# Kernel tuning notes

Measured on AMD Instinct MI355X. Metric: run time of the kernel, lower is better.

## Reference

```python
import jax, jax.numpy as jnp
import numpy as np

B, S, HID = 1, 4096, 2048
H, KVH, D = 16, 8, 128
EPS = 1e-6
SCALE = D ** -0.5


def rms_norm(x, w):
    # normalize over last axis in float32, per-head weight of size D
    xf = x.astype(jnp.float32)
    var = jnp.mean(xf * xf, axis=-1, keepdims=True)
    return (w * xf * jax.lax.rsqrt(var + EPS)).astype(x.dtype)


def rotate_half(x):
    x1, x2 = jnp.split(x, 2, axis=-1)
    return jnp.concatenate([-x2, x1], axis=-1)


def setup_inputs() -> dict:
    key = jax.random.key(0)
    ks = jax.random.split(key, 12)
    x = jax.random.normal(ks[0], (B, S, HID), jnp.float32)
    # RoPE tables
    inv_freq = 1.0 / (10000.0 ** (jnp.arange(0, D, 2, dtype=jnp.float32) / D))
    t = jnp.arange(S, dtype=jnp.float32)
    freqs = jnp.outer(t, inv_freq)                       # [S, D/2]
    emb = jnp.concatenate([freqs, freqs], axis=-1)       # [S, D]
    cos, sin = jnp.cos(emb), jnp.sin(emb)
    # causal additive mask
    neg = jnp.finfo(jnp.float32).min
    mask = jnp.where(jnp.tril(jnp.ones((S, S), bool)), 0.0, neg)[None, None]
    sc = 0.02
    Wq = jax.random.normal(ks[1], (H * D, HID), jnp.float32) * sc
    bq = jnp.zeros((H * D,), jnp.float32)
    Wk = jax.random.normal(ks[2], (KVH * D, HID), jnp.float32) * sc
    bk = jnp.zeros((KVH * D,), jnp.float32)
    Wv = jax.random.normal(ks[3], (KVH * D, HID), jnp.float32) * sc
    bv = jnp.zeros((KVH * D,), jnp.float32)
    Wo = jax.random.normal(ks[4], (HID, H * D), jnp.float32) * sc
    qn_w = jnp.ones((D,), jnp.float32)
    kn_w = jnp.ones((D,), jnp.float32)
    return {"x": x, "cos": cos, "sin": sin, "mask": mask,
            "Wq": Wq, "bq": bq, "Wk": Wk, "bk": bk, "Wv": Wv, "bv": bv,
            "Wo": Wo, "qn_w": qn_w, "kn_w": kn_w}


def reference(x, cos, sin, mask, Wq, bq, Wk, bk, Wv, bv, Wo, qn_w, kn_w):
    b, s, _ = x.shape
    q = (x @ Wq.T + bq).reshape(b, s, H, D)
    k = (x @ Wk.T + bk).reshape(b, s, KVH, D)
    v = (x @ Wv.T + bv).reshape(b, s, KVH, D)
    q = rms_norm(q, qn_w)
    k = rms_norm(k, kn_w)
    # RoPE: cos/sin [S, D] broadcast over batch and head dims
    c = cos[None, :, None, :]
    sn = sin[None, :, None, :]
    q = q * c + rotate_half(q) * sn
    k = k * c + rotate_half(k) * sn
    # GQA: repeat kv heads (repeat_interleave along head axis)
    reps = H // KVH
    k = jnp.repeat(k, reps, axis=2)
    v = jnp.repeat(v, reps, axis=2)
    # [b, H, s, d]
    q = q.transpose(0, 2, 1, 3)
    k = k.transpose(0, 2, 1, 3)
    v = v.transpose(0, 2, 1, 3)
    scores = jnp.einsum('bhqd,bhkd->bhqk', q, k) * SCALE + mask
    attn = jax.nn.softmax(scores.astype(jnp.float32), axis=-1).astype(q.dtype)
    out = jnp.einsum('bhqk,bhkd->bhqd', attn, v)
    out = out.transpose(0, 2, 1, 3).reshape(b, s, H * D)
    return out @ Wo.T
```

## Files before the change

kernel.cpp:

```cpp
#include <hip/hip_runtime.h>
#include <hip/hip_bf16.h>
#include <stdint.h>

#define S_LEN 4096
#define HID 2048
#define NH 16
#define KVH 8
#define DH 128
#define EPS 1e-6f
#define SCALE 0.08838834764831845f
#define LOG2E 1.4426950408889634f

#if __has_builtin(__builtin_amdgcn_exp2f)
#define EXP2(x) __builtin_amdgcn_exp2f(x)
#else
#define EXP2(x) exp2f(x)
#endif

typedef __bf16 bf16x8 __attribute__((ext_vector_type(8)));
typedef __bf16 bf16x4 __attribute__((ext_vector_type(4)));
typedef float f32x4 __attribute__((ext_vector_type(4)));

__device__ inline void gl_lds16(const __bf16* g, __bf16* l) {
  __builtin_amdgcn_global_load_lds(
      (const __attribute__((address_space(1))) void*)g,
      (__attribute__((address_space(3))) void*)l, 16, 0, 0);
}

__global__ __launch_bounds__(256) void f2b4(
    const float* __restrict__ in, __bf16* __restrict__ out, int n4) {
  int i = blockIdx.x * 256 + threadIdx.x;
  if (i < n4) {
    float4 v = ((const float4*)in)[i];
    bf16x4 o;
    o[0] = (__bf16)v.x; o[1] = (__bf16)v.y; o[2] = (__bf16)v.z; o[3] = (__bf16)v.w;
    ((bf16x4*)out)[i] = o;
  }
}


template <typename TC>
__global__ __launch_bounds__(256) void gemm128(
    const __bf16* __restrict__ A, const __bf16* __restrict__ B,
    const float* __restrict__ bias, TC* __restrict__ C,
    int N, int K, int bias_mode)
{
  __shared__ __attribute__((aligned(16))) __bf16 As[3][128 * 32];
  __shared__ __attribute__((aligned(16))) __bf16 Bs[3][128 * 32];
  const int wave = threadIdx.x >> 6, lane = threadIdx.x & 63;
  const int quad = lane >> 4, l16 = lane & 15;
  const int wm = wave >> 1, wn = wave & 1;
  const int m0 = blockIdx.y * 128, n0 = blockIdx.x * 128;
  const int srow = lane >> 2, scol = (lane & 3) * 8;

  auto stage = [&](int buf, int k0) {
#pragma unroll
    for (int j = wave; j < 8; j += 4) {
      gl_lds16(A + (size_t)(m0 + j * 16 + srow) * K + k0 + scol, &As[buf][j * 512]);
      gl_lds16(B + (size_t)(n0 + j * 16 + srow) * K + k0 + scol, &Bs[buf][j * 512]);
    }
  };

  f32x4 acc[4][4] = {};
  const int nk = K >> 5;
  stage(0, 0);
  stage(1, 32);

  int cur = 0, pre = 2;
  for (int kt = 0; kt < nk; ++kt) {
    if (kt + 1 < nk) asm volatile("s_waitcnt vmcnt(4)" ::: "memory");
    else             asm volatile("s_waitcnt vmcnt(0)" ::: "memory");
    __builtin_amdgcn_s_barrier();
    __builtin_amdgcn_sched_barrier(0);
    if (kt + 2 < nk) stage(pre, (kt + 2) * 32);

    bf16x8 af[4], bfr[4];
#pragma unroll
    for (int s = 0; s < 4; ++s) {
      af[s]  = *(const bf16x8*)(&As[cur][(wm * 64 + s * 16 + l16) * 32 + quad * 8]);
      bfr[s] = *(const bf16x8*)(&Bs[cur][(wn * 64 + s * 16 + l16) * 32 + quad * 8]);
    }
#pragma unroll
    for (int ms = 0; ms < 4; ++ms)
#pragma unroll
      for (int ns = 0; ns < 4; ++ns)
        acc[ms][ns] = __builtin_amdgcn_mfma_f32_16x16x32_bf16(
            af[ms], bfr[ns], acc[ms][ns], 0, 0, 0);

    cur = (cur == 2) ? 0 : cur + 1;
    pre = (pre == 2) ? 0 : pre + 1;
  }

#pragma unroll
  for (int ms = 0; ms < 4; ++ms)
#pragma unroll
    for (int ns = 0; ns < 4; ++ns)
#pragma unroll
      for (int r = 0; r < 4; ++r) {
        int row = m0 + wm * 64 + ms * 16 + quad * 4 + r;
        int col = n0 + wn * 64 + ns * 16 + l16;
        float v = acc[ms][ns][r];
        if (bias_mode == 1) v += bias[col];
        else if (bias_mode == 2) v += bias[row];
        C[(size_t)row * N + col] = (TC)v;
      }
}

__global__ __launch_bounds__(256) void gemm_qkv(
    const __bf16* __restrict__ A,
    const __bf16* __restrict__ B,
    const float* __restrict__ bq, const float* __restrict__ bk,
    const float* __restrict__ bv,
    __bf16* __restrict__ qo,
    __bf16* __restrict__ ko,
    __bf16* __restrict__ vto)
{
  __shared__ __attribute__((aligned(16))) __bf16 As[3][128 * 32];
  __shared__ __attribute__((aligned(16))) __bf16 Bs[3][128 * 32];
  const int wave = threadIdx.x >> 6, lane = threadIdx.x & 63;
  const int quad = lane >> 4, l16 = lane & 15;
  const int wm = wave >> 1, wn = wave & 1;
  const int m0 = blockIdx.y * 128, n0 = blockIdx.x * 128;
  const int srow = lane >> 2, scol = (lane & 3) * 8;
  const int K = HID;

  auto stage = [&](int buf, int k0) {
#pragma unroll
    for (int j = wave; j < 8; j += 4) {
      gl_lds16(A + (size_t)(m0 + j * 16 + srow) * K + k0 + scol, &As[buf][j * 512]);
      gl_lds16(B + (size_t)(n0 + j * 16 + srow) * K + k0 + scol, &Bs[buf][j * 512]);
    }
  };

  f32x4 acc[4][4] = {};
  const int nk = K >> 5;
  stage(0, 0);
  stage(1, 32);

  int cur = 0, pre = 2;
  for (int kt = 0; kt < nk; ++kt) {
    if (kt + 1 < nk) asm volatile("s_waitcnt vmcnt(4)" ::: "memory");
    else             asm volatile("s_waitcnt vmcnt(0)" ::: "memory");
    __builtin_amdgcn_s_barrier();
    __builtin_amdgcn_sched_barrier(0);
    if (kt + 2 < nk) stage(pre, (kt + 2) * 32);

    bf16x8 af[4], bfr[4];
#pragma unroll
    for (int s = 0; s < 4; ++s) {
      af[s]  = *(const bf16x8*)(&As[cur][(wm * 64 + s * 16 + l16) * 32 + quad * 8]);
      bfr[s] = *(const bf16x8*)(&Bs[cur][(wn * 64 + s * 16 + l16) * 32 + quad * 8]);
    }
#pragma unroll
    for (int ms = 0; ms < 4; ++ms)
#pragma unroll
      for (int ns = 0; ns < 4; ++ns)
        acc[ms][ns] = __builtin_amdgcn_mfma_f32_16x16x32_bf16(
            af[ms], bfr[ns], acc[ms][ns], 0, 0, 0);

    cur = (cur == 2) ? 0 : cur + 1;
    pre = (pre == 2) ? 0 : pre + 1;
  }

  if (blockIdx.x < 24) {
#pragma unroll
    for (int ms = 0; ms < 4; ++ms)
#pragma unroll
      for (int ns = 0; ns < 4; ++ns)
#pragma unroll
        for (int r = 0; r < 4; ++r) {
          int row = m0 + wm * 64 + ms * 16 + quad * 4 + r;
          int col = n0 + wn * 64 + ns * 16 + l16;
          float v = acc[ms][ns][r];
          if (col < 2048) { v += bq[col];        qo[(size_t)row * HID + col] = (__bf16)v; }
          else            { v += bk[col - 2048]; ko[(size_t)row * (KVH * DH) + (col - 2048)] = (__bf16)v; }
        }
  } else {
#pragma unroll
    for (int ms = 0; ms < 4; ++ms)
#pragma unroll
      for (int ns = 0; ns < 4; ++ns) {
        int vr = n0 - 3072 + wn * 64 + ns * 16 + l16;
        int s0 = m0 + wm * 64 + ms * 16 + quad * 4;
        float b = bv[vr];
        bf16x4 p;
#pragma unroll
        for (int r = 0; r < 4; ++r) p[r] = (__bf16)(acc[ms][ns][r] + b);
        *(bf16x4*)(vto + (size_t)vr * S_LEN + s0) = p;
      }
  }
}

__global__ __launch_bounds__(256) void rmsnorm_rope(
    __bf16* __restrict__ q, __bf16* __restrict__ k,
    const float* __restrict__ cosb, const float* __restrict__ sinb,
    const float* __restrict__ qw, const float* __restrict__ kw)
{
  const int wave = threadIdx.x >> 6;
  const int lane = threadIdx.x & 63;
  const int row = blockIdx.x * 4 + wave;
  const int s   = row / (NH + KVH);
  const int idx = row % (NH + KVH);

  __bf16* base;
  const float* w;
  float oscale;
  if (idx < NH) { base = q + ((size_t)s * NH + idx) * DH;         w = qw; oscale = SCALE * LOG2E; }
  else          { base = k + ((size_t)s * KVH + (idx - NH)) * DH; w = kw; oscale = 1.0f; }

  float x1 = (float)base[lane];
  float x2 = (float)base[lane + 64];
  float ss = x1 * x1 + x2 * x2;
#pragma unroll
  for (int m = 1; m < 64; m <<= 1) ss += __shfl_xor(ss, m, 64);
  float inv = rsqrtf(ss * (1.0f / 128.0f) + EPS);

  float xh1 = x1 * inv * w[lane];
  float xh2 = x2 * inv * w[lane + 64];
  const float* cs = cosb + (size_t)s * DH;
  const float* sn = sinb + (size_t)s * DH;
  base[lane]      = (__bf16)((xh1 * cs[lane]      - xh2 * sn[lane])      * oscale);
  base[lane + 64] = (__bf16)((xh2 * cs[lane + 64] + xh1 * sn[lane + 64]) * oscale);
}

__global__ __launch_bounds__(256) void attn2(
    const __bf16* __restrict__ q,
    const __bf16* __restrict__ k,
    const __bf16* __restrict__ vt,
    __bf16* __restrict__ o)
{
  __shared__ __attribute__((aligned(16))) __bf16 Ks[2][64 * DH];
  __shared__ __attribute__((aligned(16))) __bf16 Vs[2][DH * 64];
  __shared__ __attribute__((aligned(16))) __bf16 pl[4][16 * 72];
  const int wave = threadIdx.x >> 6, lane = threadIdx.x & 63;
  const int quad = lane >> 4, l16 = lane & 15;
  const int h = blockIdx.y, kvh = h >> 1;

  const __bf16* kh = k + (size_t)kvh * DH;
  const __bf16* vh = vt + (size_t)kvh * DH * S_LEN;

  int krow[4], kcol[4], vrow[4], vcol[4];
#pragma unroll
  for (int i = 0; i < 4; ++i) {
    int j = wave + i * 4;
    int r = j * 4 + (lane >> 4);
    int cbK = ((lane & 15) * 16) ^ ((r & 7) << 4);
    krow[i] = r; kcol[i] = cbK >> 1;
    int d = j * 8 + (lane >> 3);
    int cbV = ((lane & 7) * 16) ^ ((d & 7) << 4);
    vrow[i] = d; vcol[i] = cbV >> 1;
  }
  auto stage = [&](int buf, int k0) {
#pragma unroll
    for (int i = 0; i < 4; ++i)
      gl_lds16(kh + (size_t)(k0 + krow[i]) * (KVH * DH) + kcol[i],
               &Ks[buf][(wave + i * 4) * 512]);
#pragma unroll
    for (int i = 0; i < 4; ++i)
      gl_lds16(vh + (size_t)vrow[i] * S_LEN + k0 + vcol[i],
               &Vs[buf][(wave + i * 4) * 512]);
  };

  for (int phase = 0; phase < 2; ++phase) {
    const int qt = phase == 0 ? (int)blockIdx.x : 63 - (int)blockIdx.x;
    const int qbase = qt * 64 + wave * 16;

    bf16x8 qa[4];
    const __bf16* qrow = q + ((size_t)(qbase + l16) * NH + h) * DH + quad * 8;
#pragma unroll
    for (int c = 0; c < 4; ++c) qa[c] = *(const bf16x8*)(qrow + c * 32);

    f32x4 oacc[8] = {};
    float mrun[4], lrun[4];
#pragma unroll
    for (int r = 0; r < 4; ++r) { mrun[r] = -3.0e38f; lrun[r] = 0.0f; }

    __syncthreads();
    stage(0, 0);

    for (int kt = 0; kt <= qt; ++kt) {
      const int cur = kt & 1;
      const int k0 = kt * 64;
      __syncthreads();
      if (kt < qt) stage(cur ^ 1, k0 + 64);

      const char* ksb = (const char*)Ks[cur];
      const char* vsb = (const char*)Vs[cur];

      f32x4 sc[4] = {};
#pragma unroll
      for (int tt = 0; tt < 4; ++tt) {
        const int row = tt * 16 + l16;
        const int swz = (row & 7) << 4;
#pragma unroll
        for (int c = 0; c < 4; ++c) {
          bf16x8 bk = *(const bf16x8*)(ksb + row * 256 + ((c * 64 + quad * 16) ^ swz));
          sc[tt] = __builtin_amdgcn_mfma_f32_16x16x32_bf16(qa[c], bk, sc[tt], 0, 0, 0);
        }
      }
      if (kt == qt) {
#pragma unroll
        for (int tt = 0; tt < 4; ++tt)
#pragma unroll
          for (int r = 0; r < 4; ++r) {
            int col = k0 + tt * 16 + l16;
            int row = qbase + quad * 4 + r;
            if (col > row) sc[tt][r] = -3.0e38f;
          }
      }
      float pmax[4];
      bool defer = true;
#pragma unroll
      for (int r = 0; r < 4; ++r) {
        float mx = fmaxf(fmaxf(sc[0][r], sc[1][r]), fmaxf(sc[2][r], sc[3][r]));
        pmax[r] = mx;
        defer = defer && (mx - mrun[r] <= 8.0f);
      }
      if (__all(defer)) {
#pragma unroll
        for (int r = 0; r < 4; ++r) {
          float s0 = EXP2(sc[0][r] - mrun[r]);
          float s1 = EXP2(sc[1][r] - mrun[r]);
          float s2 = EXP2(sc[2][r] - mrun[r]);
          float s3 = EXP2(sc[3][r] - mrun[r]);
          sc[0][r] = s0; sc[1][r] = s1; sc[2][r] = s2; sc[3][r] = s3;
          lrun[r] += (s0 + s1) + (s2 + s3);
        }
      } else {
#pragma unroll
        for (int r = 0; r < 4; ++r) {
          float mx = pmax[r];
#pragma unroll
          for (int msk = 1; msk < 16; msk <<= 1) mx = fmaxf(mx, __shfl_xor(mx, msk, 64));
          float mnew = fmaxf(mrun[r], mx);
          float sum = 0.0f;
#pragma unroll
          for (int tt = 0; tt < 4; ++tt) {
            float p = EXP2(sc[tt][r] - mnew);
            sc[tt][r] = p;
            sum += p;
          }
          float alpha = EXP2(mrun[r] - mnew);
          lrun[r] = lrun[r] * alpha + sum;
          mrun[r] = mnew;
#pragma unroll
          for (int c = 0; c < 8; ++c) oacc[c][r] *= alpha;
        }
      }
#pragma unroll
      for (int tt = 0; tt < 4; ++tt)
#pragma unroll
        for (int r = 0; r < 4; ++r)
          pl[wave][(quad * 4 + r) * 72 + tt * 16 + l16] = (__bf16)sc[tt][r];
      bf16x8 pa[2];
#pragma unroll
      for (int kc = 0; kc < 2; ++kc)
        pa[kc] = *(const bf16x8*)(pl[wave] + l16 * 72 + kc * 32 + quad * 8);
#pragma unroll
      for (int c = 0; c < 8; ++c)
#pragma unroll
        for (int kc = 0; kc < 2; ++kc) {
          const int d = c * 16 + l16;
          bf16x8 bv = *(const bf16x8*)(
              vsb + d * 128 + ((kc * 64 + quad * 16) ^ ((d & 7) << 4)));
          oacc[c] = __builtin_amdgcn_mfma_f32_16x16x32_bf16(pa[kc], bv, oacc[c], 0, 0, 0);
        }
    }

#pragma unroll
    for (int r = 0; r < 4; ++r) {
#pragma unroll
      for (int msk = 1; msk < 16; msk <<= 1) lrun[r] += __shfl_xor(lrun[r], msk, 64);
      lrun[r] = 1.0f / lrun[r];
    }
#pragma unroll
    for (int c = 0; c < 8; ++c)
#pragma unroll
      for (int r = 0; r < 4; ++r) {
        int row = qbase + quad * 4 + r;
        o[((size_t)row * NH + h) * DH + c * 16 + l16] = (__bf16)(oacc[c][r] * lrun[r]);
      }
  }
}

extern "C" void kernel_launch(void* const* d_in, const int* in_sizes, int n_in,
                              void* d_out, int out_size, void* d_ws, size_t ws_size,
                              hipStream_t stream) {
  const float* x    = (const float*)d_in[0];
  const float* cosb = (const float*)d_in[1];
  const float* sinb = (const float*)d_in[2];
  const float* Wq  = (const float*)d_in[4];
  const float* bq  = (const float*)d_in[5];
  const float* Wk  = (const float*)d_in[6];
  const float* bk  = (const float*)d_in[7];
  const float* Wv  = (const float*)d_in[8];
  const float* bv  = (const float*)d_in[9];
  const float* Wo  = (const float*)d_in[10];
  const float* qnw = (const float*)d_in[11];
  const float* knw = (const float*)d_in[12];
  float* out = (float*)d_out;

  char* ws = (char*)d_ws;
  __bf16* xb    = (__bf16*)(ws);
  __bf16* Wqb   = (__bf16*)(ws + (16u << 20));
  __bf16* Wkb   = (__bf16*)(ws + (24u << 20));
  __bf16* Wvb   = (__bf16*)(ws + (28u << 20));
  __bf16* kbuf  = (__bf16*)(ws + (32u << 20));
  __bf16* vtbuf = (__bf16*)(ws + (40u << 20));
  __bf16* Wob   = (__bf16*)(ws + (16u << 20));
  __bf16* ao    = (__bf16*)(ws);
  __bf16* qbuf = (__bf16*)d_out;

  dim3 blk(256);
  f2b4<<<dim3(8192), blk, 0, stream>>>(x,  xb,  2097152);
  f2b4<<<dim3(4096), blk, 0, stream>>>(Wq, Wqb, 1048576);
  f2b4<<<dim3(2048), blk, 0, stream>>>(Wk, Wkb, 524288);
  f2b4<<<dim3(2048), blk, 0, stream>>>(Wv, Wvb, 524288);
  gemm_qkv<<<dim3(32, 32), blk, 0, stream>>>(
      xb, Wqb, bq, bk, bv, qbuf, kbuf, vtbuf);
  rmsnorm_rope<<<dim3(S_LEN * (NH + KVH) / 4), blk, 0, stream>>>(
      qbuf, kbuf, cosb, sinb, qnw, knw);
  f2b4<<<dim3(4096), blk, 0, stream>>>(Wo, Wob, 1048576);
  attn2<<<dim3(32, NH), blk, 0, stream>>>(qbuf, kbuf, vtbuf, ao);
  gemm128<float><<<dim3(16, 32), blk, 0, stream>>>(ao, Wob, nullptr, out, HID, HID, 0);
}
```

Baseline: 475.8 us.

## Enlarge QKV GEMM tile to 256x256 with XOR-swizzled LDS and 512 threads

Rewrites the fused QKV projection GEMM to use 256x256 output tiles, K-step 64, 8 waves per block and double buffering in place of triple buffering. LDS staging uses an XOR swizzle on the column offset to avoid bank conflicts on the fragment reads. The larger tile raises arithmetic intensity and data reuse per LDS load. In exchange the grid shrinks to 256 blocks, about one per CU, and LDS use and register pressure go up (128 KB LDS, 32 accumulators per thread).

Result: faster. 466.0 us (-2.1%).

```diff
diff --git a/kernel.cpp b/kernel.cpp
--- a/kernel.cpp
+++ b/kernel.cpp
@@ -37,7 +37,6 @@
     ((bf16x4*)out)[i] = o;
   }
 }
-
 
 template <typename TC>
 __global__ __launch_bounds__(256) void gemm128(
@@ -106,7 +105,7 @@
       }
 }
 
-__global__ __launch_bounds__(256) void gemm_qkv(
+__global__ __launch_bounds__(512) void gemm_qkv256(
     const __bf16* __restrict__ A,
     const __bf16* __restrict__ B,
     const float* __restrict__ bq, const float* __restrict__ bk,
@@ -115,77 +114,86 @@
     __bf16* __restrict__ ko,
     __bf16* __restrict__ vto)
 {
-  __shared__ __attribute__((aligned(16))) __bf16 As[3][128 * 32];
-  __shared__ __attribute__((aligned(16))) __bf16 Bs[3][128 * 32];
-  const int wave = threadIdx.x >> 6, lane = threadIdx.x & 63;
+  __shared__ __attribute__((aligned(16))) __bf16 Abuf[2][256 * 64];
+  __shared__ __attribute__((aligned(16))) __bf16 Bbuf[2][256 * 64];
+  const int tid = threadIdx.x;
+  const int wid = tid >> 6, lane = tid & 63;
   const int quad = lane >> 4, l16 = lane & 15;
-  const int wm = wave >> 1, wn = wave & 1;
-  const int m0 = blockIdx.y * 128, n0 = blockIdx.x * 128;
-  const int srow = lane >> 2, scol = (lane & 3) * 8;
+  const int wm = wid >> 2, wn = wid & 3;
+  const int m0 = blockIdx.y * 256, n0 = blockIdx.x * 256;
   const int K = HID;
 
+  const int srow  = tid >> 3;
+  const int scole = (((tid & 7) * 16) ^ ((srow & 7) << 4)) >> 1;
+
   auto stage = [&](int buf, int k0) {
 #pragma unroll
-    for (int j = wave; j < 8; j += 4) {
-      gl_lds16(A + (size_t)(m0 + j * 16 + srow) * K + k0 + scol, &As[buf][j * 512]);
-      gl_lds16(B + (size_t)(n0 + j * 16 + srow) * K + k0 + scol, &Bs[buf][j * 512]);
+    for (int c = 0; c < 4; ++c) {
+      gl_lds16(A + (size_t)(m0 + c * 64 + srow) * K + k0 + scole,
+               &Abuf[buf][c * 4096 + wid * 512]);
+      gl_lds16(B + (size_t)(n0 + c * 64 + srow) * K + k0 + scole,
+               &Bbuf[buf][c * 4096 + wid * 512]);
     }
   };
 
-  f32x4 acc[4][4] = {};
-  const int nk = K >> 5;
+  f32x4 acc[8][4] = {};
+  const int nk = K >> 6;
+  const int swz = (l16 & 7) << 4;
   stage(0, 0);
-  stage(1, 32);
-
-  int cur = 0, pre = 2;
+
   for (int kt = 0; kt < nk; ++kt) {
-    if (kt + 1 < nk) asm volatile("s_waitcnt vmcnt(4)" ::: "memory");
-    else             asm volatile("s_waitcnt vmcnt(0)" ::: "memory");
-    __builtin_amdgcn_s_barrier();
-    __builtin_amdgcn_sched_barrier(0);
-    if (kt + 2 < nk) stage(pre, (kt + 2) * 32);
-
-    bf16x8 af[4], bfr[4];
-#pragma unroll
-    for (int s = 0; s < 4; ++s) {
-      af[s]  = *(const bf16x8*)(&As[cur][(wm * 64 + s * 16 + l16) * 32 + quad * 8]);
-      bfr[s] = *(const bf16x8*)(&Bs[cur][(wn * 64 + s * 16 + l16) * 32 + quad * 8]);
-    }
-#pragma unroll
-    for (int ms = 0; ms < 4; ++ms)
-#pragma unroll
-      for (int ns = 0; ns < 4; ++ns)
-        acc[ms][ns] = __builtin_amdgcn_mfma_f32_16x16x32_bf16(
-            af[ms], bfr[ns], acc[ms][ns], 0, 0, 0);
-
-    cur = (cur == 2) ? 0 : cur + 1;
-    pre = (pre == 2) ? 0 : pre + 1;
-  }
-
-  if (blockIdx.x < 24) {
-#pragma unroll
-    for (int ms = 0; ms < 4; ++ms)
-#pragma unroll
-      for (int ns = 0; ns < 4; ++ns)
+    const int cur = kt & 1;
+    __syncthreads();
+    if (kt + 1 < nk) stage(cur ^ 1, (kt + 1) * 64);
+
+    const char* ab = (const char*)Abuf[cur];
+    const char* bb = (const char*)Bbuf[cur];
+#pragma unroll
+    for (int ks = 0; ks < 2; ++ks) {
+      bf16x8 af[8], bfr[4];
+#pragma unroll
+      for (int fr = 0; fr < 8; ++fr) {
+        int rl = wm * 128 + fr * 16 + l16;
+        af[fr] = *(const bf16x8*)(ab + rl * 128 + ((ks * 64 + quad * 16) ^ swz));
+      }
+#pragma unroll
+      for (int fn = 0; fn < 4; ++fn) {
+        int rl = wn * 64 + fn * 16 + l16;
+        bfr[fn] = *(const bf16x8*)(bb + rl * 128 + ((ks * 64 + quad * 16) ^ swz));
+      }
+#pragma unroll
+      for (int fr = 0; fr < 8; ++fr)
+#pragma unroll
+        for (int fn = 0; fn < 4; ++fn)
+          acc[fr][fn] = __builtin_amdgcn_mfma_f32_16x16x32_bf16(
+              af[fr], bfr[fn], acc[fr][fn], 0, 0, 0);
+    }
+  }
+
+  if (blockIdx.x < 12) {
+#pragma unroll
+    for (int fr = 0; fr < 8; ++fr)
+#pragma unroll
+      for (int fn = 0; fn < 4; ++fn)
 #pragma unroll
         for (int r = 0; r < 4; ++r) {
-          int row = m0 + wm * 64 + ms * 16 + quad * 4 + r;
-          int col = n0 + wn * 64 + ns * 16 + l16;
-          float v = acc[ms][ns][r];
+          int row = m0 + wm * 128 + fr * 16 + quad * 4 + r;
+          int col = n0 + wn * 64 + fn * 16 + l16;
+          float v = acc[fr][fn][r];
           if (col < 2048) { v += bq[col];        qo[(size_t)row * HID + col] = (__bf16)v; }
           else            { v += bk[col - 2048]; ko[(size_t)row * (KVH * DH) + (col - 2048)] = (__bf16)v; }
         }
   } else {
 #pragma unroll
-    for (int ms = 0; ms < 4; ++ms)
-#pragma unroll
-      for (int ns = 0; ns < 4; ++ns) {
-        int vr = n0 - 3072 + wn * 64 + ns * 16 + l16;
-        int s0 = m0 + wm * 64 + ms * 16 + quad * 4;
+    for (int fr = 0; fr < 8; ++fr)
+#pragma unroll
+      for (int fn = 0; fn < 4; ++fn) {
+        int vr = n0 - 3072 + wn * 64 + fn * 16 + l16;
+        int s0 = m0 + wm * 128 + fr * 16 + quad * 4;
         float b = bv[vr];
         bf16x4 p;
 #pragma unroll
-        for (int r = 0; r < 4; ++r) p[r] = (__bf16)(acc[ms][ns][r] + b);
+        for (int r = 0; r < 4; ++r) p[r] = (__bf16)(acc[fr][fn][r] + b);
         *(bf16x4*)(vto + (size_t)vr * S_LEN + s0) = p;
       }
   }
@@ -416,7 +424,7 @@
   f2b4<<<dim3(4096), blk, 0, stream>>>(Wq, Wqb, 1048576);
   f2b4<<<dim3(2048), blk, 0, stream>>>(Wk, Wkb, 524288);
   f2b4<<<dim3(2048), blk, 0, stream>>>(Wv, Wvb, 524288);
-  gemm_qkv<<<dim3(32, 32), blk, 0, stream>>>(
+  gemm_qkv256<<<dim3(16, 16), dim3(512), 0, stream>>>(
       xb, Wqb, bq, bk, bv, qbuf, kbuf, vtbuf);
   rmsnorm_rope<<<dim3(S_LEN * (NH + KVH) / 4), blk, 0, stream>>>(
       qbuf, kbuf, cosb, sinb, qnw, knw);
```
